# Performance work log

Hardware: AMD Instinct MI355X
Metric: run time of the kernel (lower is better)

Reference implementation:

```python
import jax, jax.numpy as jnp
import numpy as np

T = 64        # n_estimators
DEPTH = 8
D = 2**DEPTH - 1   # internal nodes per tree (255)
K = 2**DEPTH       # leaves per tree (256)
M = 512       # n_features
C = 8         # class_num
B = 4096      # batch


def _build_path_masks():
    # Complete binary tree in heap order. For leaf l, walk from root;
    # going LEFT corresponds to b==+1 -> multiply (1 - x_node) -> Bpos,
    # going RIGHT corresponds to b==-1 -> multiply x_node -> Bneg.
    Bpos = np.zeros((K, D), dtype=np.float32)
    Bneg = np.zeros((K, D), dtype=np.float32)
    for l in range(K):
        node = 0
        for level in range(DEPTH):
            bit = (l >> (DEPTH - 1 - level)) & 1
            if bit == 0:
                Bpos[l, node] = 1.0
            else:
                Bneg[l, node] = 1.0
            node = 2 * node + 1 + bit
    return Bpos, Bneg


def setup_inputs() -> dict:
    rng = np.random.default_rng(0)
    key = jax.random.key(0)
    x = jax.random.normal(key, (B, M), dtype=jnp.float32)
    # fcn1: each internal node splits on one feature -> one-hot weight row,
    # bias = -threshold (change_parameters1).
    feat = rng.integers(0, M, size=(T, D))
    W1 = np.zeros((T, D, M), dtype=np.float32)
    W1[np.arange(T)[:, None], np.arange(D)[None, :], feat] = 1.0
    b1 = (-rng.standard_normal((T, D))).astype(np.float32)  # -threshold
    # Path masks shared across trees (complete trees), tiled per tree.
    Bpos1, Bneg1 = _build_path_masks()
    Bpos = np.broadcast_to(Bpos1, (T, K, D)).copy()
    Bneg = np.broadcast_to(Bneg1, (T, K, D)).copy()
    # fcn2 weight = c^T with zero bias (change_parameters2): leaf values [T, K, C]
    Cw = rng.random((T, K, C)).astype(np.float32)
    return {
        "input": x,
        "W1": jnp.asarray(W1),
        "b1": jnp.asarray(b1),
        "Bpos": jnp.asarray(Bpos),
        "Bneg": jnp.asarray(Bneg),
        "Cw": jnp.asarray(Cw),
    }


def reference(input, W1, b1, Bpos, Bneg, Cw):
    # z: [B, T, D] = 10 * (fcn1 per tree)
    z = 10.0 * (jnp.einsum("bm,tdm->btd", input, W1) + b1)
    # x = sigmoid(z); leaf-path product:
    #   x_c[b,t,k] = prod_d x^Bneg[t,k,d] * (1-x)^Bpos[t,k,d]
    # computed exactly in log-space (all factors in (0,1)):
    log_x = jax.nn.log_sigmoid(z)       # log sigmoid(z)
    log_1mx = jax.nn.log_sigmoid(-z)    # log (1 - sigmoid(z))
    log_xc = (jnp.einsum("btd,tkd->btk", log_x, Bneg)
              + jnp.einsum("btd,tkd->btk", log_1mx, Bpos))
    x_c = jnp.exp(log_xc)               # [B, T, K]
    # fcn2 (zero bias) then forest average over trees
    out = jnp.einsum("btk,tkc->bc", x_c, Cw) / T
    return out
```

## Files before the change

### kernel.cpp

```cpp
#include <hip/hip_runtime.h>
#include <hip/hip_bf16.h>

#define TT 64
#define DD 255
#define KK 256
#define MM 512
#define CC 8
#define BB 4096
#define RB 16
#define TPB 16
#define ST 18
#define XS 16

typedef _Float16 h8 __attribute__((ext_vector_type(8)));
typedef _Float16 h2v __attribute__((ext_vector_type(2)));
typedef float f4 __attribute__((ext_vector_type(4)));
typedef uint32_t u32a __attribute__((may_alias));

__device__ __forceinline__ h2v pkrtz(float a, float b) {
    return __builtin_bit_cast(h2v, __builtin_amdgcn_cvt_pkrtz(a, b));
}

__device__ __forceinline__ float wave_sum(float v) {
    v += __shfl_down(v, 32, 64);
    v += __shfl_down(v, 16, 64);
    v += __shfl_down(v, 8, 64);
    v += __shfl_down(v, 4, 64);
    v += __shfl_down(v, 2, 64);
    v += __shfl_down(v, 1, 64);
    return v;
}

__global__ void feat_kernel(const float* __restrict__ W1, int* __restrict__ feat) {
    const int row = blockIdx.x * 4 + (threadIdx.x >> 6);
    const int lane = threadIdx.x & 63;
    const float4* r = reinterpret_cast<const float4*>(W1 + (size_t)row * MM);
    float4 a = r[lane];
    float4 b = r[lane + 64];
    float ba = (float)(4 * lane);
    float bb = (float)(4 * (lane + 64));
    float acc = 0.0f;
    acc = fmaf(a.x, ba,        acc);
    acc = fmaf(a.y, ba + 1.0f, acc);
    acc = fmaf(a.z, ba + 2.0f, acc);
    acc = fmaf(a.w, ba + 3.0f, acc);
    acc = fmaf(b.x, bb,        acc);
    acc = fmaf(b.y, bb + 1.0f, acc);
    acc = fmaf(b.z, bb + 2.0f, acc);
    acc = fmaf(b.w, bb + 3.0f, acc);
    acc = wave_sum(acc);
    if (lane == 0) feat[row] = (int)(acc + 0.5f);
}

__global__ void cwt_kernel(const float* __restrict__ Cw, _Float16* __restrict__ cwT) {
    int idx = blockIdx.x * 256 + threadIdx.x;
    int t = idx >> 8, k = idx & 255;
    int c = k >> 5, sl = (k >> 3) & 3, j = k & 7;
    const float4* p = reinterpret_cast<const float4*>(Cw + (size_t)idx * CC);
    float4 p0 = p[0], p1 = p[1];
    _Float16* base = cwT + ((((t * 8 + c) * 8) * 4 + sl) * 8 + j);
    base[0 * 32] = (_Float16)p0.x;
    base[1 * 32] = (_Float16)p0.y;
    base[2 * 32] = (_Float16)p0.z;
    base[3 * 32] = (_Float16)p0.w;
    base[4 * 32] = (_Float16)p1.x;
    base[5 * 32] = (_Float16)p1.y;
    base[6 * 32] = (_Float16)p1.z;
    base[7 * 32] = (_Float16)p1.w;
}

__device__ __forceinline__ float sigm_from(float xv, float c1) {
    float earg = fmaf(-14.426950408889634f, xv, c1);
    float e = exp2f(earg);
    return __builtin_amdgcn_rcpf(1.0f + e);
}

__global__ __launch_bounds__(256, 2) void forest_kernel(
        const float* __restrict__ x, const float* __restrict__ b1,
        const _Float16* __restrict__ cwT, const int* __restrict__ feat,
        float* __restrict__ out) {
    __shared__ __align__(16) _Float16 xsi[MM * XS];
    __shared__ _Float16 s8[4][256 * ST];

    const int tid = threadIdx.x;
    const int w = tid >> 6;
    const int lane = tid & 63;
    const int b0 = blockIdx.x * RB;
    const int t0 = blockIdx.y * TPB;
    const int m = lane & 15;
    const int slot = lane >> 4;

    for (int idx = tid; idx < MM * RB; idx += 256) {
        int mm = idx & (MM - 1);
        int r = idx >> 9;
        xsi[mm * XS + r] = (_Float16)x[(size_t)(b0 + r) * MM + mm];
    }
    __syncthreads();

    _Float16* s8w = s8[w];

    const int b3 = slot >> 1, b4 = slot & 1;
    const float sg3 = (float)(2 * b3 - 1), off3 = (float)(1 - b3);
    const float sg4 = (float)(2 * b4 - 1), off4 = (float)(1 - b4);

    f4 acc = {0.f, 0.f, 0.f, 0.f};

    auto ldmeta = [&](int t, int kq, int& f, float& c1) {
        int d = kq * 64 + lane;
        int idx = t * DD + (d < DD ? d : 0);
        f = feat[idx];
        c1 = -14.426950408889634f * b1[idx];
    };

    int fcur[4]; float ccur[4];
    #pragma unroll
    for (int kq = 0; kq < 4; ++kq) ldmeta(t0 + w * 4, kq, fcur[kq], ccur[kq]);

    #pragma unroll
    for (int tt = 0; tt < 4; ++tt) {
        const int t = t0 + w * 4 + tt;

        asm volatile("" ::: "memory");

        h8 bfr[8] = {};
        if (m < CC) {
            const h8* cp = reinterpret_cast<const h8*>(cwT) +
                           (((t * 8 + 0) * 8 + m) * 4 + slot);
            #pragma unroll
            for (int c = 0; c < 8; ++c) bfr[c] = cp[c * 32];
        }

        int fnxt[4]; float cnxt[4];
        #pragma unroll
        for (int kq = 0; kq < 4; ++kq) { fnxt[kq] = fcur[kq]; cnxt[kq] = ccur[kq]; }
        if (tt < 3) {
            #pragma unroll
            for (int kq = 0; kq < 4; ++kq) ldmeta(t + 1, kq, fnxt[kq], cnxt[kq]);
        }

        #pragma unroll
        for (int kq = 0; kq < 4; ++kq) {
            int d = kq * 64 + lane;
            if (d < DD) {
                const float4* xp = reinterpret_cast<const float4*>(xsi + fcur[kq] * XS);
                float4 A = xp[0], Bv = xp[1];
                float c1 = ccur[kq];
                u32a* sp = reinterpret_cast<u32a*>(s8w + d * ST);
                uint32_t raw[8] = {
                    __builtin_bit_cast(uint32_t, A.x), __builtin_bit_cast(uint32_t, A.y),
                    __builtin_bit_cast(uint32_t, A.z), __builtin_bit_cast(uint32_t, A.w),
                    __builtin_bit_cast(uint32_t, Bv.x), __builtin_bit_cast(uint32_t, Bv.y),
                    __builtin_bit_cast(uint32_t, Bv.z), __builtin_bit_cast(uint32_t, Bv.w)};
                #pragma unroll
                for (int i2 = 0; i2 < 8; ++i2) {
                    h2v u = __builtin_bit_cast(h2v, raw[i2]);
                    float sa = sigm_from((float)u.x, c1);
                    float sb = sigm_from((float)u.y, c1);
                    sp[i2] = __builtin_bit_cast(uint32_t, pkrtz(sa, sb));
                }
            }
        }
        asm volatile("s_waitcnt lgkmcnt(0)" ::: "memory");

        float s0 = (float)s8w[0 * ST + m];
        float s1 = (float)s8w[1 * ST + m];
        float s2 = (float)s8w[2 * ST + m];
        float s3 = (float)s8w[3 * ST + m];
        float s4 = (float)s8w[4 * ST + m];
        float s5p = (float)s8w[5 * ST + m];
        float s6 = (float)s8w[6 * ST + m];
        float P10 = 1.0f - s0, P11 = s0;
        float P200 = P10 * (1.0f - s1), P201 = P10 * s1;
        float P210 = P11 * (1.0f - s2), P211 = P11 * s2;
        float P3a[8];
        P3a[0] = P200 * (1.0f - s3); P3a[1] = P200 * s3;
        P3a[2] = P201 * (1.0f - s4); P3a[3] = P201 * s4;
        P3a[4] = P210 * (1.0f - s5p); P3a[5] = P210 * s5p;
        P3a[6] = P211 * (1.0f - s6); P3a[7] = P211 * s6;

        #pragma unroll
        for (int c = 0; c < 8; ++c) {
            const int n3 = 7 + c;
            float sc3 = (float)s8w[n3 * ST + m];
            float f3 = fmaf(sg3, sc3, off3);
            int n4 = 2 * n3 + 1 + b3;
            float sc4 = (float)s8w[n4 * ST + m];
            float f4v = fmaf(sg4, sc4, off4);
            float P5 = P3a[c] * f3 * f4v;
            int n5 = 2 * n4 + 1 + b4;
            float s5 = (float)s8w[n5 * ST + m];
            float v1 = P5 * s5, v0 = P5 - v1;
            int q0 = 2 * n5 + 1;
            float sq0 = (float)s8w[q0 * ST + m];
            float sq1 = (float)s8w[(q0 + 1) * ST + m];
            float w01 = v0 * sq0, w00 = v0 - w01;
            float w11 = v1 * sq1, w10 = v1 - w11;
            int r0 = 2 * q0 + 1;
            float sr0 = (float)s8w[(r0 + 0) * ST + m];
            float sr1 = (float)s8w[(r0 + 1) * ST + m];
            float sr2 = (float)s8w[(r0 + 2) * ST + m];
            float sr3 = (float)s8w[(r0 + 3) * ST + m];
            float l1 = w00 * sr0, l0 = w00 - l1;
            float l3 = w01 * sr1, l2 = w01 - l3;
            float l5 = w10 * sr2, l4 = w10 - l5;
            float l7 = w11 * sr3, l6 = w11 - l7;
            union { h8 v; h2v p[4]; } U;
            U.p[0] = pkrtz(l0, l1);
            U.p[1] = pkrtz(l2, l3);
            U.p[2] = pkrtz(l4, l5);
            U.p[3] = pkrtz(l6, l7);
            acc = __builtin_amdgcn_mfma_f32_16x16x32_f16(U.v, bfr[c], acc, 0, 0, 0);
        }

        #pragma unroll
        for (int kq = 0; kq < 4; ++kq) { fcur[kq] = fnxt[kq]; ccur[kq] = cnxt[kq]; }
    }

    __syncthreads();
    f4* red = reinterpret_cast<f4*>(xsi);
    red[w * 64 + lane] = acc;
    __syncthreads();
    if (tid < 64) {
        f4 sum = red[0 * 64 + tid];
        sum += red[1 * 64 + tid];
        sum += red[2 * 64 + tid];
        sum += red[3 * 64 + tid];
        int n = tid & 15, sl = tid >> 4;
        if (n < CC) {
            #pragma unroll
            for (int reg = 0; reg < 4; ++reg) {
                int row = sl * 4 + reg;
                atomicAdd(&out[(size_t)(b0 + row) * CC + n], sum[reg] * (1.0f / 64.0f));
            }
        }
    }
}

extern "C" void kernel_launch(void* const* d_in, const int* in_sizes, int n_in,
                              void* d_out, int out_size, void* d_ws, size_t ws_size,
                              hipStream_t stream) {
    const float* x  = (const float*)d_in[0];
    const float* W1 = (const float*)d_in[1];
    const float* b1 = (const float*)d_in[2];
    const float* Cw = (const float*)d_in[5];
    float* out = (float*)d_out;

    _Float16* cwT = (_Float16*)d_ws;
    int* feat = (int*)((char*)d_ws + (size_t)TT * KK * CC * sizeof(_Float16));

    (void)hipMemsetAsync(out, 0, (size_t)BB * CC * sizeof(float), stream);
    feat_kernel<<<(TT * DD) / 4, 256, 0, stream>>>(W1, feat);
    cwt_kernel<<<(TT * KK) / 256, 256, 0, stream>>>(Cw, cwT);
    forest_kernel<<<dim3(BB / RB, TT / TPB), 256, 0, stream>>>(x, b1, cwT, feat, out);
}
```

Measured before the change: 141.7 us.

## Compute last-level node sigmoids inline instead of staging them in shared memory

The sigmoid table is now built only for the first 127 nodes of each tree. The 128 last-level split values are computed on the fly inside the leaf/MFMA loop, using per-lane feature and threshold metadata prepacked by a new small kernel. This halves the shared-memory footprint and the per-tree staging writes, and drops the padded lanes of the fourth quarter. In exchange it adds global metadata loads and scattered LDS reads of x inside the inner loop, plus one extra kernel launch.

```diff
diff --git a/kernel.cpp b/kernel.cpp
--- a/kernel.cpp
+++ b/kernel.cpp
@@ -69,6 +69,18 @@
     base[7 * 32] = (_Float16)p1.w;
 }
 
+__global__ void meta7_kernel(const int* __restrict__ feat, const float* __restrict__ b1,
+                             int4* __restrict__ m7f, float4* __restrict__ m7c) {
+    int idx = blockIdx.x * 256 + threadIdx.x;
+    if (idx >= TT * 32) return;
+    int t = idx >> 5, rem = idx & 31;
+    int c = rem >> 2, sg = rem & 3;
+    int r0 = t * DD + 127 + 16 * c + 4 * sg;
+    m7f[idx] = make_int4(feat[r0], feat[r0 + 1], feat[r0 + 2], feat[r0 + 3]);
+    const float K1 = -14.426950408889634f;
+    m7c[idx] = make_float4(K1 * b1[r0], K1 * b1[r0 + 1], K1 * b1[r0 + 2], K1 * b1[r0 + 3]);
+}
+
 __device__ __forceinline__ float sigm_from(float xv, float c1) {
     float earg = fmaf(-14.426950408889634f, xv, c1);
     float e = exp2f(earg);
@@ -78,9 +90,10 @@
 __global__ __launch_bounds__(256, 2) void forest_kernel(
         const float* __restrict__ x, const float* __restrict__ b1,
         const _Float16* __restrict__ cwT, const int* __restrict__ feat,
+        const int4* __restrict__ m7f, const float4* __restrict__ m7c,
         float* __restrict__ out) {
     __shared__ __align__(16) _Float16 xsi[MM * XS];
-    __shared__ _Float16 s8[4][256 * ST];
+    __shared__ _Float16 s8[4][128 * ST];
 
     const int tid = threadIdx.x;
     const int w = tid >> 6;
@@ -107,14 +120,14 @@
 
     auto ldmeta = [&](int t, int kq, int& f, float& c1) {
         int d = kq * 64 + lane;
-        int idx = t * DD + (d < DD ? d : 0);
+        int idx = t * DD + (d < 127 ? d : 0);
         f = feat[idx];
         c1 = -14.426950408889634f * b1[idx];
     };
 
-    int fcur[4]; float ccur[4];
+    int fcur[2]; float ccur[2];
     #pragma unroll
-    for (int kq = 0; kq < 4; ++kq) ldmeta(t0 + w * 4, kq, fcur[kq], ccur[kq]);
+    for (int kq = 0; kq < 2; ++kq) ldmeta(t0 + w * 4, kq, fcur[kq], ccur[kq]);
 
     #pragma unroll
     for (int tt = 0; tt < 4; ++tt) {
@@ -130,18 +143,18 @@
             for (int c = 0; c < 8; ++c) bfr[c] = cp[c * 32];
         }
 
-        int fnxt[4]; float cnxt[4];
-        #pragma unroll
-        for (int kq = 0; kq < 4; ++kq) { fnxt[kq] = fcur[kq]; cnxt[kq] = ccur[kq]; }
+        int fnxt[2]; float cnxt[2];
+        #pragma unroll
+        for (int kq = 0; kq < 2; ++kq) { fnxt[kq] = fcur[kq]; cnxt[kq] = ccur[kq]; }
         if (tt < 3) {
             #pragma unroll
-            for (int kq = 0; kq < 4; ++kq) ldmeta(t + 1, kq, fnxt[kq], cnxt[kq]);
-        }
-
-        #pragma unroll
-        for (int kq = 0; kq < 4; ++kq) {
+            for (int kq = 0; kq < 2; ++kq) ldmeta(t + 1, kq, fnxt[kq], cnxt[kq]);
+        }
+
+        #pragma unroll
+        for (int kq = 0; kq < 2; ++kq) {
             int d = kq * 64 + lane;
-            if (d < DD) {
+            if (d < 127) {
                 const float4* xp = reinterpret_cast<const float4*>(xsi + fcur[kq] * XS);
                 float4 A = xp[0], Bv = xp[1];
                 float c1 = ccur[kq];
@@ -195,11 +208,13 @@
             float sq1 = (float)s8w[(q0 + 1) * ST + m];
             float w01 = v0 * sq0, w00 = v0 - w01;
             float w11 = v1 * sq1, w10 = v1 - w11;
-            int r0 = 2 * q0 + 1;
-            float sr0 = (float)s8w[(r0 + 0) * ST + m];
-            float sr1 = (float)s8w[(r0 + 1) * ST + m];
-            float sr2 = (float)s8w[(r0 + 2) * ST + m];
-            float sr3 = (float)s8w[(r0 + 3) * ST + m];
+            int midx = (t * 8 + c) * 4 + slot;
+            int4 fr = m7f[midx];
+            float4 cr = m7c[midx];
+            float sr0 = sigm_from((float)xsi[fr.x * XS + m], cr.x);
+            float sr1 = sigm_from((float)xsi[fr.y * XS + m], cr.y);
+            float sr2 = sigm_from((float)xsi[fr.z * XS + m], cr.z);
+            float sr3 = sigm_from((float)xsi[fr.w * XS + m], cr.w);
             float l1 = w00 * sr0, l0 = w00 - l1;
             float l3 = w01 * sr1, l2 = w01 - l3;
             float l5 = w10 * sr2, l4 = w10 - l5;
@@ -213,7 +228,7 @@
         }
 
         #pragma unroll
-        for (int kq = 0; kq < 4; ++kq) { fcur[kq] = fnxt[kq]; ccur[kq] = cnxt[kq]; }
+        for (int kq = 0; kq < 2; ++kq) { fcur[kq] = fnxt[kq]; ccur[kq] = cnxt[kq]; }
     }
 
     __syncthreads();
@@ -245,11 +260,15 @@
     const float* Cw = (const float*)d_in[5];
     float* out = (float*)d_out;
 
-    _Float16* cwT = (_Float16*)d_ws;
-    int* feat = (int*)((char*)d_ws + (size_t)TT * KK * CC * sizeof(_Float16));
+    char* wsb = (char*)d_ws;
+    _Float16* cwT = (_Float16*)wsb;
+    int* feat = (int*)(wsb + 262144);
+    int4* m7f = (int4*)(wsb + 262144 + 65536);
+    float4* m7c = (float4*)(wsb + 262144 + 65536 + 32768);
 
     (void)hipMemsetAsync(out, 0, (size_t)BB * CC * sizeof(float), stream);
     feat_kernel<<<(TT * DD) / 4, 256, 0, stream>>>(W1, feat);
     cwt_kernel<<<(TT * KK) / 256, 256, 0, stream>>>(Cw, cwT);
-    forest_kernel<<<dim3(BB / RB, TT / TPB), 256, 0, stream>>>(x, b1, cwT, feat, out);
-}
+    meta7_kernel<<<(TT * 32 + 255) / 256, 256, 0, stream>>>(feat, b1, m7f, m7c);
+    forest_kernel<<<dim3(BB / RB, TT / TPB), 256, 0, stream>>>(x, b1, cwT, feat, m7f, m7c, out);
+}
```

Measured after the change: 144.0 us. No clear change (+1.6%).
